# Optimization experiments

Measured on AMD Instinct MI355X. Metric: run time of the kernel, lower is better.

Reference implementation:

```python
import jax, jax.numpy as jnp
import numpy as np

CH = 64  # channels
QK = CH // 8  # query/key projection dim


def setup_inputs() -> dict:
    key = jax.random.key(0)
    ks = jax.random.split(key, 8)
    B, C, H, W = 4, CH, 64, 64
    s = 1.0 / np.sqrt(C)
    x = jax.random.normal(ks[0], (B, C, H, W), dtype=jnp.float32)
    Wq = jax.random.normal(ks[1], (QK, C), dtype=jnp.float32) * s
    bq = jnp.zeros((QK,), dtype=jnp.float32)
    Wk = jax.random.normal(ks[2], (QK, C), dtype=jnp.float32) * s
    bk = jnp.zeros((QK,), dtype=jnp.float32)
    Wv = jax.random.normal(ks[3], (C, C), dtype=jnp.float32) * s
    bv = jnp.zeros((C,), dtype=jnp.float32)
    gamma = jnp.zeros((1,), dtype=jnp.float32)
    return {"x": x, "Wq": Wq, "bq": bq, "Wk": Wk, "bk": bk,
            "Wv": Wv, "bv": bv, "gamma": gamma}


def reference(x, Wq, bq, Wk, bk, Wv, bv, gamma):
    B, C, H, W = x.shape
    # 1x1 convs == per-pixel linear projections over channels
    q = jnp.einsum('bchw,dc->bdhw', x, Wq) + bq[None, :, None, None]
    k = jnp.einsum('bchw,dc->bdhw', x, Wk) + bk[None, :, None, None]
    v = jnp.einsum('bchw,dc->bdhw', x, Wv) + bv[None, :, None, None]
    q = q.reshape(B, -1, H * W)             # [B, QK, HW]
    k = k.reshape(B, -1, H * W)             # [B, QK, HW]
    v = v.reshape(B, C, H * W)              # [B, C, HW]
    # attention[b, i, j] = <q[:, i], k[:, j]>, softmax over j (last dim)
    attn = jax.nn.softmax(jnp.einsum('bdi,bdj->bij', q, k), axis=-1)
    # out = value @ attention^T  -> out[b, c, i] = sum_j v[b,c,j] * attn[b,i,j]
    out = jnp.einsum('bcj,bij->bci', v, attn).reshape(B, C, H, W)
    return gamma[0] * out + x
```

## Files before the change

### kernel.cpp

```cpp
#include <hip/hip_runtime.h>
#include <hip/hip_bf16.h>
#include <stdint.h>

typedef float f32x4 __attribute__((ext_vector_type(4)));
typedef short s16x8 __attribute__((ext_vector_type(8)));
typedef unsigned short u16;
typedef uint8_t u8;

#define LOG2E 1.44269504088896340736f
#define FP8MAX 448.0f

#if __has_builtin(__builtin_amdgcn_exp2f)
#define EXP2F __builtin_amdgcn_exp2f
#else
#define EXP2F exp2f
#endif

__device__ __forceinline__ u16 f2bf(float f) {
    union { float f; uint32_t u; } v; v.f = f;
    uint32_t r = v.u + 0x7FFFu + ((v.u >> 16) & 1u);
    return (u16)(r >> 16);
}
__device__ __forceinline__ uint32_t cvt2bf(float lo, float hi) {
    __hip_bfloat162 h = __float22bfloat162_rn(float2{lo, hi});
    union { __hip_bfloat162 h; uint32_t u; } v; v.h = h; return v.u;
}
__device__ __forceinline__ float bflo2f(uint32_t u) {
    union { uint32_t u; float f; } v; v.u = u << 16; return v.f;
}
__device__ __forceinline__ float bfhi2f(uint32_t u) {
    union { uint32_t u; float f; } v; v.u = u & 0xffff0000u; return v.f;
}
__device__ __forceinline__ uint32_t cvt4fp8(float a, float b, float c, float d) {
    int w = __builtin_amdgcn_cvt_pk_fp8_f32(a, b, 0, false);
    w     = __builtin_amdgcn_cvt_pk_fp8_f32(c, d, w, true);
    return (uint32_t)w;
}
__device__ __forceinline__ void ds_write16(u8* d, uint4 v) {
    uint2 lo; lo.x = v.x; lo.y = v.y;
    uint2 hi; hi.x = v.z; hi.y = v.w;
    *(uint2*)(d)     = lo;
    *(uint2*)(d + 8) = hi;
}
__device__ __forceinline__ void lds_barrier() {
    asm volatile("s_waitcnt lgkmcnt(0)\n\ts_barrier" ::: "memory");
}

__global__ __launch_bounds__(256) void qkv_kernel(
    const float* __restrict__ x,
    const float* __restrict__ Wq, const float* __restrict__ bq,
    const float* __restrict__ Wk, const float* __restrict__ bk,
    const float* __restrict__ Wv, const float* __restrict__ bv,
    u16* __restrict__ QT, u16* __restrict__ KT, u8* __restrict__ Vg)
{
    const int tid  = threadIdx.x;
    const int lane = tid & 63;
    const int wave = tid >> 6;
    const int blk  = blockIdx.x;
    const int b    = blk >> 8;
    const int sub  = blk & 255;
    const int jt   = sub >> 2;
    const int cg   = sub & 3;
    const int j    = (jt << 6) + lane;

    const float* xb = x + (size_t)b * 64 * 4096 + j;
    float xv[64];
#pragma unroll
    for (int c = 0; c < 64; ++c) xv[c] = xb[(size_t)c * 4096];

#pragma unroll
    for (int co = 0; co < 4; ++co) {
        const int row = __builtin_amdgcn_readfirstlane(cg * 16 + wave * 4 + co);
        const float* wrow = Wv + row * 64;
        float acc = bv[row];
#pragma unroll
        for (int cin = 0; cin < 64; ++cin) acc += wrow[cin] * xv[cin];
        acc = fminf(fmaxf(acc, -FP8MAX), FP8MAX);
        Vg[((size_t)(b * 64 + row)) * 4096 + j] =
            (u8)(__builtin_amdgcn_cvt_pk_fp8_f32(acc, acc, 0, false) & 0xff);
    }

    if (cg == 0) {
        if (wave == 0) {
            union { u16 u[8]; uint4 v; } q;
#pragma unroll
            for (int d = 0; d < 8; ++d) {
                const float* wrow = Wq + d * 64;
                float acc = bq[d];
#pragma unroll
                for (int cin = 0; cin < 64; ++cin) acc += wrow[cin] * xv[cin];
                q.u[d] = f2bf(acc * LOG2E);
            }
            *(uint4*)(QT + ((size_t)b * 4096 + j) * 8) = q.v;
        } else if (wave == 1) {
            union { u16 u[8]; uint4 v; } k;
#pragma unroll
            for (int d = 0; d < 8; ++d) {
                const float* wrow = Wk + d * 64;
                float acc = bk[d];
#pragma unroll
                for (int cin = 0; cin < 64; ++cin) acc += wrow[cin] * xv[cin];
                k.u[d] = f2bf(acc);
            }
            *(uint4*)(KT + ((size_t)b * 4096 + j) * 8) = k.v;
        }
    }
}

#define P_STRIDE 72
#define VROW 72
#define OXW 65

__global__ __launch_bounds__(1024, 4) void attn_kernel(
    const u16* __restrict__ QT, const u16* __restrict__ KT,
    const u8* __restrict__ Vg, const float* __restrict__ x,
    const float* __restrict__ gamma, float* __restrict__ out)
{
    __shared__ alignas(16) u8 p_lds[16][2][16 * P_STRIDE];
    __shared__ alignas(16) u8 vbuf[4][2][64 * VROW];
    __shared__ uint32_t OxP[12][8 * OXW];
    __shared__ float    Lx[12 * 16];

    const int tid  = threadIdx.x;
    const int lane = tid & 63;
    const int wave = tid >> 6;
    const int col  = lane & 15;
    const int quad = lane >> 4;
    const int qg   = wave & 3;
    const int sp   = wave >> 2;
    const int blk  = blockIdx.x;
    const int b    = blk >> 6;
    const int i0   = (blk & 63) << 6;
    const int iw   = i0 + qg * 16;

    const u16* KTb = KT + (size_t)b * 4096 * 8;
    const u8*  Vb  = Vg + (size_t)b * 64 * 4096;

    const s16x8 z8 = {0,0,0,0,0,0,0,0};
    const f32x4 zero = {0.f, 0.f, 0.f, 0.f};

    s16x8 aq = z8;
    if (quad == 0)
        aq = *(const s16x8*)(QT + ((size_t)b * 4096 + iw + col) * 8);

    f32x4 o[4];
#pragma unroll
    for (int nt = 0; nt < 4; ++nt) o[nt] = zero;
    float lsum = 0.f;

    u8* plA = &p_lds[wave][0][0];
    u8* plB = &p_lds[wave][1][0];

    const int srow = (qg << 4) + (lane >> 2);
    const int schk = lane & 3;
    const u8* vsrc = Vb + (size_t)srow * 4096 + schk * 16;
    u8* vdst0 = &vbuf[sp][0][srow * VROW + schk * 16];
    u8* vdst1 = &vbuf[sp][1][srow * VROW + schk * 16];

    const int jbeg = sp << 10;

    s16x8 kb[4];
#pragma unroll
    for (int nt = 0; nt < 4; ++nt) {
        s16x8 kn = z8;
        if (quad == 0)
            kn = *(const s16x8*)(KTb + (size_t)(jbeg + nt * 16 + col) * 8);
        kb[nt] = kn;
    }
    ds_write16(vdst0, *(const uint4*)(vsrc + jbeg));

    long long ap0 = 0, ap1 = 0;

#pragma unroll 2
    for (int t = 0; t < 16; ++t) {
        const int j0 = jbeg + (t << 6);
        u8* plw = (t & 1) ? plB : plA;
        u8* plr = (t & 1) ? plA : plB;

        uint4 vstg;
        if (t < 15) vstg = *(const uint4*)(vsrc + j0 + 64);

        if (t > 0) {
            ap0 = *(const long long*)(plr + col * P_STRIDE + quad * 8);
            ap1 = *(const long long*)(plr + col * P_STRIDE + 32 + quad * 8);
        }

        f32x4 s[4];
#pragma unroll
        for (int nt = 0; nt < 4; ++nt)
            s[nt] = __builtin_amdgcn_mfma_f32_16x16x32_bf16(kb[nt], aq, zero, 0, 0, 0);

        if (t < 15) {
#pragma unroll
            for (int nt = 0; nt < 4; ++nt) {
                s16x8 kn = z8;
                if (quad == 0)
                    kn = *(const s16x8*)(KTb + (size_t)(j0 + 64 + nt * 16 + col) * 8);
                kb[nt] = kn;
            }
        }

#pragma unroll
        for (int nt = 0; nt < 4; ++nt) {
            float p0 = fminf(EXP2F(s[nt][0]), FP8MAX);
            float p1 = fminf(EXP2F(s[nt][1]), FP8MAX);
            float p2 = fminf(EXP2F(s[nt][2]), FP8MAX);
            float p3 = fminf(EXP2F(s[nt][3]), FP8MAX);
            lsum += (p0 + p1) + (p2 + p3);
            *(uint32_t*)(plw + col * P_STRIDE + nt * 16 + quad * 4) =
                cvt4fp8(p0, p1, p2, p3);
        }
        asm volatile("" ::: "memory");

        if (t > 0) {
            const u8* vt = &vbuf[sp][(t - 1) & 1][0];
#pragma unroll
            for (int nt = 0; nt < 4; ++nt) {
                long long b0 = *(const long long*)(vt + (nt * 16 + col) * VROW + quad * 8);
                long long b1 = *(const long long*)(vt + (nt * 16 + col) * VROW + quad * 8 + 32);
                o[nt] = __builtin_amdgcn_mfma_f32_16x16x32_fp8_fp8(ap0, b0, o[nt], 0, 0, 0);
                o[nt] = __builtin_amdgcn_mfma_f32_16x16x32_fp8_fp8(ap1, b1, o[nt], 0, 0, 0);
            }
        }

        lds_barrier();

        if (t < 15) ds_write16((t & 1) ? vdst0 : vdst1, vstg);
    }

    {
        ap0 = *(const long long*)(plB + col * P_STRIDE + quad * 8);
        ap1 = *(const long long*)(plB + col * P_STRIDE + 32 + quad * 8);
        const u8* vt = &vbuf[sp][1][0];
#pragma unroll
        for (int nt = 0; nt < 4; ++nt) {
            long long b0 = *(const long long*)(vt + (nt * 16 + col) * VROW + quad * 8);
            long long b1 = *(const long long*)(vt + (nt * 16 + col) * VROW + quad * 8 + 32);
            o[nt] = __builtin_amdgcn_mfma_f32_16x16x32_fp8_fp8(ap0, b0, o[nt], 0, 0, 0);
            o[nt] = __builtin_amdgcn_mfma_f32_16x16x32_fp8_fp8(ap1, b1, o[nt], 0, 0, 0);
        }
    }

    lsum += __shfl_xor(lsum, 16, 64);
    lsum += __shfl_xor(lsum, 32, 64);

    if (sp > 0) {
        const int slice = (sp - 1) * 4 + qg;
        uint32_t* ox = &OxP[slice][0];
#pragma unroll
        for (int nt = 0; nt < 4; ++nt) {
#pragma unroll
            for (int rp = 0; rp < 2; ++rp)
                ox[(quad * 2 + rp) * OXW + nt * 16 + col] =
                    cvt2bf(o[nt][2 * rp], o[nt][2 * rp + 1]);
        }
        if (quad == 0) Lx[slice * 16 + col] = lsum;
    }
    __syncthreads();
    if (sp == 0) {
        float ltot = lsum;
#pragma unroll
        for (int s = 0; s < 3; ++s)
            ltot += Lx[(s * 4 + qg) * 16 + col];
        float linv[4];
#pragma unroll
        for (int r = 0; r < 4; ++r)
            linv[r] = 1.0f / __shfl(ltot, quad * 4 + r, 16);

#pragma unroll
        for (int s = 0; s < 3; ++s) {
            const uint32_t* ox = &OxP[s * 4 + qg][0];
#pragma unroll
            for (int nt = 0; nt < 4; ++nt) {
#pragma unroll
                for (int rp = 0; rp < 2; ++rp) {
                    uint32_t u = ox[(quad * 2 + rp) * OXW + nt * 16 + col];
                    o[nt][2 * rp]     += bflo2f(u);
                    o[nt][2 * rp + 1] += bfhi2f(u);
                }
            }
        }
        const float g = gamma[0];
#pragma unroll
        for (int nt = 0; nt < 4; ++nt) {
            const int c = nt * 16 + col;
#pragma unroll
            for (int r = 0; r < 4; ++r) {
                const int i = iw + quad * 4 + r;
                const size_t idx = ((size_t)(b * 64 + c)) * 4096 + i;
                out[idx] = g * (o[nt][r] * linv[r]) + x[idx];
            }
        }
    }
}

extern "C" void kernel_launch(void* const* d_in, const int* in_sizes, int n_in,
                              void* d_out, int out_size, void* d_ws, size_t ws_size,
                              hipStream_t stream)
{
    const float* x     = (const float*)d_in[0];
    const float* Wq    = (const float*)d_in[1];
    const float* bq    = (const float*)d_in[2];
    const float* Wk    = (const float*)d_in[3];
    const float* bk    = (const float*)d_in[4];
    const float* Wv    = (const float*)d_in[5];
    const float* bv    = (const float*)d_in[6];
    const float* gamma = (const float*)d_in[7];

    u16* QT = (u16*)d_ws;
    u16* KT = QT + (size_t)4 * 4096 * 8;
    u8*  Vg = (u8*)(KT + (size_t)4 * 4096 * 8);

    qkv_kernel<<<1024, 256, 0, stream>>>(x, Wq, bq, Wk, bk, Wv, bv, QT, KT, Vg);
    attn_kernel<<<256, 1024, 0, stream>>>(QT, KT, Vg, x, gamma, (float*)d_out);
}
```

Baseline: 104.4 us.

## Halve attention block size to 32 query rows, doubling grid to 512 blocks

Each attention block now handles 32 query rows with 8 waves (2 query groups × 4 key splits) instead of 64 rows with 16 waves. The grid doubles to 512 blocks to fill more CUs, and each thread stages 32 bytes of V per tile instead of 16. An extra barrier after the initial V store is added. The cost is that each V tile in LDS is reused by fewer query rows, so more global V traffic per output.

```diff
diff --git a/kernel.cpp b/kernel.cpp
--- a/kernel.cpp
+++ b/kernel.cpp
@@ -111,27 +111,27 @@
 #define VROW 72
 #define OXW 65
 
-__global__ __launch_bounds__(1024, 4) void attn_kernel(
+__global__ __launch_bounds__(512, 4) void attn_kernel(
     const u16* __restrict__ QT, const u16* __restrict__ KT,
     const u8* __restrict__ Vg, const float* __restrict__ x,
     const float* __restrict__ gamma, float* __restrict__ out)
 {
-    __shared__ alignas(16) u8 p_lds[16][2][16 * P_STRIDE];
+    __shared__ alignas(16) u8 p_lds[8][2][16 * P_STRIDE];
     __shared__ alignas(16) u8 vbuf[4][2][64 * VROW];
-    __shared__ uint32_t OxP[12][8 * OXW];
-    __shared__ float    Lx[12 * 16];
+    __shared__ uint32_t OxP[6][8 * OXW];
+    __shared__ float    Lx[6 * 16];
 
     const int tid  = threadIdx.x;
     const int lane = tid & 63;
     const int wave = tid >> 6;
     const int col  = lane & 15;
     const int quad = lane >> 4;
-    const int qg   = wave & 3;
-    const int sp   = wave >> 2;
+    const int qg   = wave & 1;
+    const int sp   = wave >> 1;
     const int blk  = blockIdx.x;
-    const int b    = blk >> 6;
-    const int i0   = (blk & 63) << 6;
-    const int iw   = i0 + qg * 16;
+    const int b    = blk >> 7;
+    const int it   = blk & 127;
+    const int iw   = (it << 5) + qg * 16;
 
     const u16* KTb = KT + (size_t)b * 4096 * 8;
     const u8*  Vb  = Vg + (size_t)b * 64 * 4096;
@@ -151,11 +151,12 @@
     u8* plA = &p_lds[wave][0][0];
     u8* plB = &p_lds[wave][1][0];
 
-    const int srow = (qg << 4) + (lane >> 2);
-    const int schk = lane & 3;
-    const u8* vsrc = Vb + (size_t)srow * 4096 + schk * 16;
-    u8* vdst0 = &vbuf[sp][0][srow * VROW + schk * 16];
-    u8* vdst1 = &vbuf[sp][1][srow * VROW + schk * 16];
+    const int sidx = qg * 64 + lane;
+    const int srow = sidx >> 1;
+    const int poff = (sidx & 1) * 32;
+    const u8* vsrc = Vb + (size_t)srow * 4096 + poff;
+    u8* vdst0 = &vbuf[sp][0][srow * VROW + poff];
+    u8* vdst1 = &vbuf[sp][1][srow * VROW + poff];
 
     const int jbeg = sp << 10;
 
@@ -167,7 +168,9 @@
             kn = *(const s16x8*)(KTb + (size_t)(jbeg + nt * 16 + col) * 8);
         kb[nt] = kn;
     }
-    ds_write16(vdst0, *(const uint4*)(vsrc + jbeg));
+    ds_write16(vdst0,      *(const uint4*)(vsrc + jbeg));
+    ds_write16(vdst0 + 16, *(const uint4*)(vsrc + jbeg + 16));
+    lds_barrier();
 
     long long ap0 = 0, ap1 = 0;
 
@@ -177,8 +180,11 @@
         u8* plw = (t & 1) ? plB : plA;
         u8* plr = (t & 1) ? plA : plB;
 
-        uint4 vstg;
-        if (t < 15) vstg = *(const uint4*)(vsrc + j0 + 64);
+        uint4 vstg0, vstg1;
+        if (t < 15) {
+            vstg0 = *(const uint4*)(vsrc + j0 + 64);
+            vstg1 = *(const uint4*)(vsrc + j0 + 80);
+        }
 
         if (t > 0) {
             ap0 = *(const long long*)(plr + col * P_STRIDE + quad * 8);
@@ -225,7 +231,11 @@
 
         lds_barrier();
 
-        if (t < 15) ds_write16((t & 1) ? vdst0 : vdst1, vstg);
+        if (t < 15) {
+            u8* vd = (t & 1) ? vdst0 : vdst1;
+            ds_write16(vd,      vstg0);
+            ds_write16(vd + 16, vstg1);
+        }
     }
 
     {
@@ -245,7 +255,7 @@
     lsum += __shfl_xor(lsum, 32, 64);
 
     if (sp > 0) {
-        const int slice = (sp - 1) * 4 + qg;
+        const int slice = (sp - 1) * 2 + qg;
         uint32_t* ox = &OxP[slice][0];
 #pragma unroll
         for (int nt = 0; nt < 4; ++nt) {
@@ -261,7 +271,7 @@
         float ltot = lsum;
 #pragma unroll
         for (int s = 0; s < 3; ++s)
-            ltot += Lx[(s * 4 + qg) * 16 + col];
+            ltot += Lx[(s * 2 + qg) * 16 + col];
         float linv[4];
 #pragma unroll
         for (int r = 0; r < 4; ++r)
@@ -269,7 +279,7 @@
 
 #pragma unroll
         for (int s = 0; s < 3; ++s) {
-            const uint32_t* ox = &OxP[s * 4 + qg][0];
+            const uint32_t* ox = &OxP[s * 2 + qg][0];
 #pragma unroll
             for (int nt = 0; nt < 4; ++nt) {
 #pragma unroll
@@ -312,5 +322,5 @@
     u8*  Vg = (u8*)(KT + (size_t)4 * 4096 * 8);
 
     qkv_kernel<<<1024, 256, 0, stream>>>(x, Wq, bq, Wk, bk, Wv, bv, QT, KT, Vg);
-    attn_kernel<<<256, 1024, 0, stream>>>(QT, KT, Vg, x, gamma, (float*)d_out);
-}
+    attn_kernel<<<512, 512, 0, stream>>>(QT, KT, Vg, x, gamma, (float*)d_out);
+}
```

After: 105.8 us. About the same (+1.3%).

## Keep softmax probabilities in registers by permuting key order to match MFMA layout

Applied to the files above, without the earlier changes.

Permutes the key rows loaded per tile so the S-MFMA output fragment directly matches the A-operand layout of the fp8 PV MFMA. The per-wave P staging buffer in LDS, its writes and reads, and the one-tile software lag are removed, so PV now consumes the current tile's V after the barrier. This saves LDS traffic and shared memory but gives up the skew that overlapped exp/convert with the previous tile's PV MFMAs.

```diff
diff --git a/kernel.cpp b/kernel.cpp
--- a/kernel.cpp
+++ b/kernel.cpp
@@ -107,7 +107,6 @@
     }
 }
 
-#define P_STRIDE 72
 #define VROW 72
 #define OXW 65
 
@@ -116,7 +115,6 @@
     const u8* __restrict__ Vg, const float* __restrict__ x,
     const float* __restrict__ gamma, float* __restrict__ out)
 {
-    __shared__ alignas(16) u8 p_lds[16][2][16 * P_STRIDE];
     __shared__ alignas(16) u8 vbuf[4][2][64 * VROW];
     __shared__ uint32_t OxP[12][8 * OXW];
     __shared__ float    Lx[12 * 16];
@@ -139,6 +137,8 @@
     const s16x8 z8 = {0,0,0,0,0,0,0,0};
     const f32x4 zero = {0.f, 0.f, 0.f, 0.f};
 
+    const int pcol = ((col & 12) << 1) + (col & 3);
+
     s16x8 aq = z8;
     if (quad == 0)
         aq = *(const s16x8*)(QT + ((size_t)b * 4096 + iw + col) * 8);
@@ -147,9 +147,6 @@
 #pragma unroll
     for (int nt = 0; nt < 4; ++nt) o[nt] = zero;
     float lsum = 0.f;
-
-    u8* plA = &p_lds[wave][0][0];
-    u8* plB = &p_lds[wave][1][0];
 
     const int srow = (qg << 4) + (lane >> 2);
     const int schk = lane & 3;
@@ -164,26 +161,18 @@
     for (int nt = 0; nt < 4; ++nt) {
         s16x8 kn = z8;
         if (quad == 0)
-            kn = *(const s16x8*)(KTb + (size_t)(jbeg + nt * 16 + col) * 8);
+            kn = *(const s16x8*)(KTb +
+                (size_t)(jbeg + ((nt >> 1) << 5) + ((nt & 1) << 2) + pcol) * 8);
         kb[nt] = kn;
     }
     ds_write16(vdst0, *(const uint4*)(vsrc + jbeg));
-
-    long long ap0 = 0, ap1 = 0;
 
 #pragma unroll 2
     for (int t = 0; t < 16; ++t) {
         const int j0 = jbeg + (t << 6);
-        u8* plw = (t & 1) ? plB : plA;
-        u8* plr = (t & 1) ? plA : plB;
 
         uint4 vstg;
         if (t < 15) vstg = *(const uint4*)(vsrc + j0 + 64);
-
-        if (t > 0) {
-            ap0 = *(const long long*)(plr + col * P_STRIDE + quad * 8);
-            ap1 = *(const long long*)(plr + col * P_STRIDE + 32 + quad * 8);
-        }
 
         f32x4 s[4];
 #pragma unroll
@@ -195,11 +184,13 @@
             for (int nt = 0; nt < 4; ++nt) {
                 s16x8 kn = z8;
                 if (quad == 0)
-                    kn = *(const s16x8*)(KTb + (size_t)(j0 + 64 + nt * 16 + col) * 8);
+                    kn = *(const s16x8*)(KTb +
+                        (size_t)(j0 + 64 + ((nt >> 1) << 5) + ((nt & 1) << 2) + pcol) * 8);
                 kb[nt] = kn;
             }
         }
 
+        uint32_t w[4];
 #pragma unroll
         for (int nt = 0; nt < 4; ++nt) {
             float p0 = fminf(EXP2F(s[nt][0]), FP8MAX);
@@ -207,13 +198,15 @@
             float p2 = fminf(EXP2F(s[nt][2]), FP8MAX);
             float p3 = fminf(EXP2F(s[nt][3]), FP8MAX);
             lsum += (p0 + p1) + (p2 + p3);
-            *(uint32_t*)(plw + col * P_STRIDE + nt * 16 + quad * 4) =
-                cvt4fp8(p0, p1, p2, p3);
-        }
-        asm volatile("" ::: "memory");
-
-        if (t > 0) {
-            const u8* vt = &vbuf[sp][(t - 1) & 1][0];
+            w[nt] = cvt4fp8(p0, p1, p2, p3);
+        }
+        const long long ap0 = (long long)(((uint64_t)w[1] << 32) | w[0]);
+        const long long ap1 = (long long)(((uint64_t)w[3] << 32) | w[2]);
+
+        lds_barrier();
+
+        {
+            const u8* vt = &vbuf[sp][t & 1][0];
 #pragma unroll
             for (int nt = 0; nt < 4; ++nt) {
                 long long b0 = *(const long long*)(vt + (nt * 16 + col) * VROW + quad * 8);
@@ -223,22 +216,7 @@
             }
         }
 
-        lds_barrier();
-
         if (t < 15) ds_write16((t & 1) ? vdst0 : vdst1, vstg);
-    }
-
-    {
-        ap0 = *(const long long*)(plB + col * P_STRIDE + quad * 8);
-        ap1 = *(const long long*)(plB + col * P_STRIDE + 32 + quad * 8);
-        const u8* vt = &vbuf[sp][1][0];
-#pragma unroll
-        for (int nt = 0; nt < 4; ++nt) {
-            long long b0 = *(const long long*)(vt + (nt * 16 + col) * VROW + quad * 8);
-            long long b1 = *(const long long*)(vt + (nt * 16 + col) * VROW + quad * 8 + 32);
-            o[nt] = __builtin_amdgcn_mfma_f32_16x16x32_fp8_fp8(ap0, b0, o[nt], 0, 0, 0);
-            o[nt] = __builtin_amdgcn_mfma_f32_16x16x32_fp8_fp8(ap1, b1, o[nt], 0, 0, 0);
-        }
     }
 
     lsum += __shfl_xor(lsum, 16, 64);
```

New measurement: 102.5 us. About the same (-1.9%).
